# Kernel tuning notes

Measured on AMD Instinct MI355X. Metric: run time of the kernel, lower is better.

## Reference

```python
import jax, jax.numpy as jnp
import numpy as np

B, NODES, VOCAB, EMB, GIN_DIM, E_PER = 4096, 32, 100, 64, 64, 512
N = B * NODES            # total nodes in batched graph
LN_EPS = 1e-5


def setup_inputs() -> dict:
    key = jax.random.key(0)
    ks = jax.random.split(key, 12)
    x = jax.random.randint(ks[0], (B, NODES - 1), 0, VOCAB)
    los = jax.random.randint(ks[1], (B,), 0, 37)
    # intra-graph edges with per-graph node offsets -> flat batched edge_index [2, B*E_PER]
    src = jax.random.randint(ks[2], (B, E_PER), 0, NODES)
    dst = jax.random.randint(ks[3], (B, E_PER), 0, NODES)
    off = (jnp.arange(B) * NODES)[:, None]
    edge_index = jnp.stack([(src + off).reshape(-1), (dst + off).reshape(-1)])

    def w(k, shape, fan_in):
        return jax.random.normal(k, shape, dtype=jnp.float32) / np.float32(np.sqrt(fan_in))

    emb_tables = w(ks[4], (NODES, VOCAB, EMB), 1.0)  # one table per node/column
    win1 = w(ks[5], (EMB, GIN_DIM), EMB); bin1 = jnp.zeros((GIN_DIM,), jnp.float32)
    gin_g = jnp.ones((GIN_DIM,), jnp.float32); gin_b = jnp.zeros((GIN_DIM,), jnp.float32)
    win2 = w(ks[6], (GIN_DIM, GIN_DIM), GIN_DIM); bin2 = jnp.zeros((GIN_DIM,), jnp.float32)
    # hidden GIN MLP is SHARED across hidden layers (torch code reuses one nn.Sequential)
    wh1 = w(ks[7], (GIN_DIM, GIN_DIM), GIN_DIM); bh1 = jnp.zeros((GIN_DIM,), jnp.float32)
    gh_g = jnp.ones((GIN_DIM,), jnp.float32); gh_b = jnp.zeros((GIN_DIM,), jnp.float32)
    wh2 = w(ks[8], (GIN_DIM, GIN_DIM), GIN_DIM); bh2 = jnp.zeros((GIN_DIM,), jnp.float32)
    eps = jnp.zeros((3,), jnp.float32)  # trainable eps per layer, init 0
    cdim = GIN_DIM * 3
    wc1 = w(ks[9], (cdim, cdim * 2), cdim); bc1 = jnp.zeros((cdim * 2,), jnp.float32)
    wc2 = w(ks[10], (cdim * 2, 1), cdim * 2); bc2 = jnp.zeros((1,), jnp.float32)
    return dict(x=x, los=los, edge_index=edge_index, emb_tables=emb_tables,
                win1=win1, bin1=bin1, gin_g=gin_g, gin_b=gin_b, win2=win2, bin2=bin2,
                wh1=wh1, bh1=bh1, gh_g=gh_g, gh_b=gh_b, wh2=wh2, bh2=bh2,
                eps=eps, wc1=wc1, bc1=bc1, wc2=wc2, bc2=bc2)


def _ln(z, g, b):
    mu = z.mean(-1, keepdims=True)
    var = ((z - mu) ** 2).mean(-1, keepdims=True)
    return (z - mu) * jax.lax.rsqrt(var + LN_EPS) * g + b


def _gin_layer(h, src, dst, eps, W1, b1, g, be, W2, b2):
    # sum-aggregate neighbors: out_i = (1+eps)*h_i + sum_{(j,i) in E} h_j
    agg = jax.ops.segment_sum(h[src], dst, num_segments=N)
    z = (1.0 + eps) * h + agg
    z = jax.nn.relu(_ln(z @ W1 + b1, g, be))
    return z @ W2 + b2


def reference(x, los, edge_index, emb_tables, win1, bin1, gin_g, gin_b, win2, bin2,
              wh1, bh1, gh_g, gh_b, wh2, bh2, eps, wc1, bc1, wc2, bc2):
    xf = jnp.concatenate([x, los[:, None]], axis=1)        # [B, NODES]
    h = emb_tables[jnp.arange(NODES)[None, :], xf]         # per-column embedding lookup -> [B, NODES, EMB]
    h = h.reshape(N, EMB)
    src, dst = edge_index[0], edge_index[1]
    h1 = _gin_layer(h, src, dst, eps[0], win1, bin1, gin_g, gin_b, win2, bin2)
    h2 = _gin_layer(h1, src, dst, eps[1], wh1, bh1, gh_g, gh_b, wh2, bh2)
    h3 = _gin_layer(h2, src, dst, eps[2], wh1, bh1, gh_g, gh_b, wh2, bh2)
    pooled = jnp.concatenate([t.reshape(B, NODES, -1).sum(axis=1) for t in (h1, h2, h3)], axis=1)  # [B, 192]
    return jax.nn.relu(pooled @ wc1 + bc1) @ wc2 + bc2     # [B, 1]
```

## Files before the change

### kernel.cpp

```cpp
#include <hip/hip_runtime.h>

#define NBATCH 4096
#define NNODE  32
#define NVOCAB 100
#define DIM    64
#define EPG    512
#define HSTR   68
#define LN_EPS 1e-5f
#define CDIM   192
#define C2DIM  384

#define WS_WFRAG_OFF   0
#define WS_WC1_OFF     65536
#define WS_POOL_OFF    360448

typedef float          f32x4  __attribute__((ext_vector_type(4)));
typedef unsigned int   u32x4  __attribute__((ext_vector_type(4)));
typedef __bf16         bf16x8 __attribute__((ext_vector_type(8)));

__device__ __forceinline__ float4 ldg4(const float* __restrict__ p) {
    return *reinterpret_cast<const float4*>(p);
}
__device__ __forceinline__ unsigned short f2bf(float f) {
    return __builtin_bit_cast(unsigned short, static_cast<__bf16>(f));
}
__device__ __forceinline__ float bf2f(unsigned short h) {
    return static_cast<float>(__builtin_bit_cast(__bf16, h));
}
__device__ __forceinline__ unsigned int pk2(float a, float b) {
    return (unsigned int)f2bf(a) | ((unsigned int)f2bf(b) << 16);
}
__device__ __forceinline__ unsigned int pk2lo(float a, float b, unsigned int hi) {
    const float ra = a - bf2f((unsigned short)(hi & 0xffff));
    const float rb = b - bf2f((unsigned short)(hi >> 16));
    return pk2(ra, rb);
}
__device__ __forceinline__ bf16x8 as_bf(u32x4 v) {
    return __builtin_bit_cast(bf16x8, v);
}
#define MFMA(a, b, c) __builtin_amdgcn_mfma_f32_16x16x32_bf16(as_bf(a), as_bf(b), (c), 0, 0, 0)

extern "C" __global__ void __launch_bounds__(256)
prep_w_kernel(const float* __restrict__ win1, const float* __restrict__ win2,
              const float* __restrict__ wh1,  const float* __restrict__ wh2,
              const float* __restrict__ wc1,
              unsigned short* __restrict__ wsb, unsigned short* __restrict__ wc1f)
{
    const int blk = blockIdx.x;
    if (blk < 4) {
        const float* Ws[4] = {win1, win2, wh1, wh2};
        const float* W = Ws[blk];
        unsigned short* hi = wsb + blk * 8192;
        unsigned short* lo = hi + 4096;
        for (int f = threadIdx.x; f < 512; f += 256) {
            const int s = f >> 8, n = (f >> 6) & 3, l = f & 63;
            const int g = l >> 4, c = l & 15, col = n * 16 + c;
            unsigned int uh[4], ul[4];
            #pragma unroll
            for (int j2 = 0; j2 < 4; ++j2) {
                const float a = W[(s * 32 + g * 8 + j2 * 2)     * DIM + col];
                const float b = W[(s * 32 + g * 8 + j2 * 2 + 1) * DIM + col];
                uh[j2] = pk2(a, b);
                ul[j2] = pk2lo(a, b, uh[j2]);
            }
            *(u32x4*)(hi + f * 8) = (u32x4){uh[0], uh[1], uh[2], uh[3]};
            *(u32x4*)(lo + f * 8) = (u32x4){ul[0], ul[1], ul[2], ul[3]};
        }
    } else {
        unsigned short* hi = wc1f;
        unsigned short* lo = wc1f + 6 * 24 * 64 * 8;
        const int base = (blk - 4) * 768;
        for (int i = 0; i < 3; ++i) {
            const int e = base + i * 256 + threadIdx.x;
            const int s = e / (24 * 64), rem = e % (24 * 64);
            const int n = rem >> 6, l = rem & 63;
            const int col = n * 16 + (l & 15);
            const int k0 = s * 32 + (l >> 4) * 8;
            unsigned int uh[4], ul[4];
            #pragma unroll
            for (int j2 = 0; j2 < 4; ++j2) {
                const float a = wc1[(k0 + j2 * 2)     * C2DIM + col];
                const float b = wc1[(k0 + j2 * 2 + 1) * C2DIM + col];
                uh[j2] = pk2(a, b);
                ul[j2] = pk2lo(a, b, uh[j2]);
            }
            *(u32x4*)(hi + e * 8) = (u32x4){uh[0], uh[1], uh[2], uh[3]};
            *(u32x4*)(lo + e * 8) = (u32x4){ul[0], ul[1], ul[2], ul[3]};
        }
    }
}

extern "C" __global__ void __launch_bounds__(256, 4)
gin_fused_kernel(const int* __restrict__ x, const int* __restrict__ los,
                 const int* __restrict__ eidx,
                 const float* __restrict__ emb,
                 const float* __restrict__ bin1,
                 const float* __restrict__ gin_g, const float* __restrict__ gin_b,
                 const float* __restrict__ bin2,
                 const float* __restrict__ bh1,
                 const float* __restrict__ gh_g, const float* __restrict__ gh_b,
                 const float* __restrict__ bh2,
                 const float* __restrict__ epsv,
                 const unsigned short* __restrict__ wsb,
                 float* __restrict__ pooled_ws)
{
    __shared__ __align__(16) float S[4 * NNODE * HSTR];

    const int t  = threadIdx.x;
    const int wv = t >> 6;
    const int l  = t & 63;
    const int b  = blockIdx.x * 4 + wv;
    float* scr = &S[wv * NNODE * HSTR];
    const int lc = l & 15;
    const int lg = l >> 4;

    int* cnt = (int*)scr;
    #pragma unroll
    for (int i = 0; i < 16; ++i) cnt[l + 64 * i] = 0;
    {
        const int ebase = b * EPG;
        const int goff  = b * NNODE;
        #pragma unroll
        for (int i = 0; i < 8; ++i) {
            const int e = ebase + l + 64 * i;
            const int sN = eidx[e] - goff;
            const int dN = eidx[NBATCH * EPG + e] - goff;
            atomicAdd(&cnt[dN * NNODE + sN], 1);
        }
    }
    u32x4 adjf[2];
    #pragma unroll
    for (int m = 0; m < 2; ++m) {
        const int4 a0 = *(const int4*)&cnt[(m * 16 + lc) * NNODE + lg * 8];
        const int4 a1 = *(const int4*)&cnt[(m * 16 + lc) * NNODE + lg * 8 + 4];
        adjf[m] = (u32x4){ pk2((float)a0.x, (float)a0.y), pk2((float)a0.z, (float)a0.w),
                           pk2((float)a1.x, (float)a1.y), pk2((float)a1.z, (float)a1.w) };
    }
    {
        const int node = l >> 1;
        const int idx = (node < NNODE - 1) ? x[b * (NNODE - 1) + node] : los[b];
        const float* er = emb + ((size_t)(node * NVOCAB + idx)) * DIM + (l & 1) * 32;
        float* sr = scr + node * HSTR + (l & 1) * 32;
        #pragma unroll
        for (int i = 0; i < 8; ++i)
            *reinterpret_cast<float4*>(sr + i * 4) = ldg4(er + i * 4);
    }

    f32x4 acc[2][4];
    u32x4 azh[2][2], azl[2][2];

    for (int ly = 0; ly < 3; ++ly) {
        const float* B1 = ly ? bh1  : bin1;
        const float* Gg = ly ? gh_g : gin_g;
        const float* Gb = ly ? gh_b : gin_b;
        const float* B2 = ly ? bh2  : bin2;
        const unsigned short* W1f = wsb + (ly ? 2 : 0) * 8192;
        const unsigned short* W2f = wsb + (ly ? 3 : 1) * 8192;
        const float sc = 1.0f + epsv[ly];

        #pragma unroll
        for (int m = 0; m < 2; ++m)
            #pragma unroll
            for (int n = 0; n < 4; ++n)
                #pragma unroll
                for (int r = 0; r < 4; ++r)
                    acc[m][n][r] = sc * scr[(m * 16 + lg * 4 + r) * HSTR + n * 16 + lc];
        #pragma unroll
        for (int n = 0; n < 4; ++n) {
            float h[8];
            #pragma unroll
            for (int j = 0; j < 8; ++j) h[j] = scr[(lg * 8 + j) * HSTR + n * 16 + lc];
            u32x4 hh = (u32x4){ pk2(h[0],h[1]), pk2(h[2],h[3]), pk2(h[4],h[5]), pk2(h[6],h[7]) };
            u32x4 hl = (u32x4){ pk2lo(h[0],h[1],hh[0]), pk2lo(h[2],h[3],hh[1]),
                                pk2lo(h[4],h[5],hh[2]), pk2lo(h[6],h[7],hh[3]) };
            #pragma unroll
            for (int m = 0; m < 2; ++m) {
                acc[m][n] = MFMA(adjf[m], hh, acc[m][n]);
                acc[m][n] = MFMA(adjf[m], hl, acc[m][n]);
            }
        }

        #pragma unroll
        for (int m = 0; m < 2; ++m)
            #pragma unroll
            for (int n = 0; n < 4; ++n)
                #pragma unroll
                for (int r = 0; r < 4; ++r)
                    scr[(m * 16 + lg * 4 + r) * HSTR + n * 16 + lc] = acc[m][n][r];
        #pragma unroll
        for (int m = 0; m < 2; ++m)
            #pragma unroll
            for (int s = 0; s < 2; ++s) {
                const float4 v0 = *(const float4*)&scr[(m * 16 + lc) * HSTR + s * 32 + lg * 8];
                const float4 v1 = *(const float4*)&scr[(m * 16 + lc) * HSTR + s * 32 + lg * 8 + 4];
                azh[m][s] = (u32x4){ pk2(v0.x,v0.y), pk2(v0.z,v0.w), pk2(v1.x,v1.y), pk2(v1.z,v1.w) };
                azl[m][s] = (u32x4){ pk2lo(v0.x,v0.y,azh[m][s][0]), pk2lo(v0.z,v0.w,azh[m][s][1]),
                                     pk2lo(v1.x,v1.y,azh[m][s][2]), pk2lo(v1.z,v1.w,azh[m][s][3]) };
            }
        #pragma unroll
        for (int m = 0; m < 2; ++m)
            #pragma unroll
            for (int n = 0; n < 4; ++n)
                acc[m][n] = (f32x4){0.f, 0.f, 0.f, 0.f};
        #pragma unroll
        for (int n = 0; n < 4; ++n)
            #pragma unroll
            for (int s = 0; s < 2; ++s) {
                const u32x4 wh = *(const u32x4*)(W1f +        ((s * 4 + n) * 64 + l) * 8);
                const u32x4 wl = *(const u32x4*)(W1f + 4096 + ((s * 4 + n) * 64 + l) * 8);
                #pragma unroll
                for (int m = 0; m < 2; ++m) {
                    acc[m][n] = MFMA(azh[m][s], wh, acc[m][n]);
                    acc[m][n] = MFMA(azh[m][s], wl, acc[m][n]);
                    acc[m][n] = MFMA(azl[m][s], wh, acc[m][n]);
                }
            }

        {
            float bv[4], gg[4], gb[4];
            #pragma unroll
            for (int n = 0; n < 4; ++n) { bv[n] = B1[n * 16 + lc]; gg[n] = Gg[n * 16 + lc]; gb[n] = Gb[n * 16 + lc]; }
            #pragma unroll
            for (int m = 0; m < 2; ++m)
                #pragma unroll
                for (int r = 0; r < 4; ++r) {
                    float a0 = acc[m][0][r] + bv[0], a1 = acc[m][1][r] + bv[1];
                    float a2 = acc[m][2][r] + bv[2], a3 = acc[m][3][r] + bv[3];
                    float s1 = a0 + a1 + a2 + a3;
                    float s2 = a0 * a0 + a1 * a1 + a2 * a2 + a3 * a3;
                    s1 += __shfl_xor(s1, 1); s1 += __shfl_xor(s1, 2);
                    s1 += __shfl_xor(s1, 4); s1 += __shfl_xor(s1, 8);
                    s2 += __shfl_xor(s2, 1); s2 += __shfl_xor(s2, 2);
                    s2 += __shfl_xor(s2, 4); s2 += __shfl_xor(s2, 8);
                    const float mu  = s1 * (1.0f / 64.0f);
                    const float var = s2 * (1.0f / 64.0f) - mu * mu;
                    const float inv = rsqrtf(var + LN_EPS);
                    acc[m][0][r] = fmaxf((a0 - mu) * inv * gg[0] + gb[0], 0.f);
                    acc[m][1][r] = fmaxf((a1 - mu) * inv * gg[1] + gb[1], 0.f);
                    acc[m][2][r] = fmaxf((a2 - mu) * inv * gg[2] + gb[2], 0.f);
                    acc[m][3][r] = fmaxf((a3 - mu) * inv * gg[3] + gb[3], 0.f);
                }
        }

        #pragma unroll
        for (int m = 0; m < 2; ++m)
            #pragma unroll
            for (int n = 0; n < 4; ++n)
                #pragma unroll
                for (int r = 0; r < 4; ++r)
                    scr[(m * 16 + lg * 4 + r) * HSTR + n * 16 + lc] = acc[m][n][r];
        #pragma unroll
        for (int m = 0; m < 2; ++m)
            #pragma unroll
            for (int s = 0; s < 2; ++s) {
                const float4 v0 = *(const float4*)&scr[(m * 16 + lc) * HSTR + s * 32 + lg * 8];
                const float4 v1 = *(const float4*)&scr[(m * 16 + lc) * HSTR + s * 32 + lg * 8 + 4];
                azh[m][s] = (u32x4){ pk2(v0.x,v0.y), pk2(v0.z,v0.w), pk2(v1.x,v1.y), pk2(v1.z,v1.w) };
                azl[m][s] = (u32x4){ pk2lo(v0.x,v0.y,azh[m][s][0]), pk2lo(v0.z,v0.w,azh[m][s][1]),
                                     pk2lo(v1.x,v1.y,azh[m][s][2]), pk2lo(v1.z,v1.w,azh[m][s][3]) };
            }
        #pragma unroll
        for (int m = 0; m < 2; ++m)
            #pragma unroll
            for (int n = 0; n < 4; ++n)
                acc[m][n] = (f32x4){0.f, 0.f, 0.f, 0.f};
        #pragma unroll
        for (int n = 0; n < 4; ++n)
            #pragma unroll
            for (int s = 0; s < 2; ++s) {
                const u32x4 wh = *(const u32x4*)(W2f +        ((s * 4 + n) * 64 + l) * 8);
                const u32x4 wl = *(const u32x4*)(W2f + 4096 + ((s * 4 + n) * 64 + l) * 8);
                #pragma unroll
                for (int m = 0; m < 2; ++m) {
                    acc[m][n] = MFMA(azh[m][s], wh, acc[m][n]);
                    acc[m][n] = MFMA(azh[m][s], wl, acc[m][n]);
                    acc[m][n] = MFMA(azl[m][s], wh, acc[m][n]);
                }
            }
        #pragma unroll
        for (int n = 0; n < 4; ++n) {
            const float bb = B2[n * 16 + lc];
            #pragma unroll
            for (int m = 0; m < 2; ++m)
                #pragma unroll
                for (int r = 0; r < 4; ++r)
                    acc[m][n][r] += bb;
        }
        #pragma unroll
        for (int m = 0; m < 2; ++m)
            #pragma unroll
            for (int n = 0; n < 4; ++n)
                #pragma unroll
                for (int r = 0; r < 4; ++r)
                    scr[(m * 16 + lg * 4 + r) * HSTR + n * 16 + lc] = acc[m][n][r];
        #pragma unroll
        for (int n = 0; n < 4; ++n) {
            float p = 0.f;
            #pragma unroll
            for (int m = 0; m < 2; ++m)
                #pragma unroll
                for (int r = 0; r < 4; ++r) p += acc[m][n][r];
            p += __shfl_xor(p, 16);
            p += __shfl_xor(p, 32);
            if (l < 16)
                pooled_ws[(size_t)b * CDIM + ly * DIM + n * 16 + l] = p;
        }
    }
}

extern "C" __global__ void __launch_bounds__(256)
classifier_kernel(const float* __restrict__ pooled_ws,
                  const unsigned short* __restrict__ wc1f,
                  const float* __restrict__ bc1, const float* __restrict__ wc2,
                  const float* __restrict__ bc2, float* __restrict__ out)
{
    #define PSTR 196
    __shared__ __align__(16) float P[16 * PSTR];
    __shared__ __align__(16) unsigned int afh[6 * 64 * 4];
    __shared__ __align__(16) unsigned int afl[6 * 64 * 4];
    __shared__ float rsum[4][16];

    const int b = blockIdx.x;
    const int t = threadIdx.x;
    const int l = t & 63;
    const int w = t >> 6;
    const unsigned short* wc1lo = wc1f + 73728;

    for (int i = t; i < 16 * 48; i += 256) {
        const int row = i / 48, q = i % 48;
        const float4 v = ldg4(pooled_ws + ((size_t)(b * 16 + row)) * CDIM + q * 4);
        *reinterpret_cast<float4*>(&P[row * PSTR + q * 4]) = v;
    }
    __syncthreads();

    for (int e = t; e < 6 * 64; e += 256) {
        const int s = e >> 6, ll = e & 63;
        const int row = ll & 15;
        const int k0 = s * 32 + (ll >> 4) * 8;
        const float4 v0 = *reinterpret_cast<const float4*>(&P[row * PSTR + k0]);
        const float4 v1 = *reinterpret_cast<const float4*>(&P[row * PSTR + k0 + 4]);
        const float y[8] = { v0.x, v0.y, v0.z, v0.w, v1.x, v1.y, v1.z, v1.w };
        unsigned int uh[4], ul[4];
        #pragma unroll
        for (int j2 = 0; j2 < 4; ++j2) {
            uh[j2] = pk2(y[j2 * 2], y[j2 * 2 + 1]);
            ul[j2] = pk2lo(y[j2 * 2], y[j2 * 2 + 1], uh[j2]);
        }
        *reinterpret_cast<u32x4*>(&afh[e * 4]) = (u32x4){uh[0], uh[1], uh[2], uh[3]};
        *reinterpret_cast<u32x4*>(&afl[e * 4]) = (u32x4){ul[0], ul[1], ul[2], ul[3]};
    }
    __syncthreads();

    float part[4] = {0.f, 0.f, 0.f, 0.f};
    for (int nt = 0; nt < 6; ++nt) {
        const int n = w * 6 + nt;
        f32x4 acc = {0.f, 0.f, 0.f, 0.f};
        #pragma unroll
        for (int s = 0; s < 6; ++s) {
            const u32x4 ah = *(const u32x4*)&afh[(s * 64 + l) * 4];
            const u32x4 al = *(const u32x4*)&afl[(s * 64 + l) * 4];
            const u32x4 bh = *(const u32x4*)&wc1f [((s * 24 + n) * 64 + l) * 8];
            const u32x4 bl = *(const u32x4*)&wc1lo[((s * 24 + n) * 64 + l) * 8];
            acc = MFMA(ah, bh, acc);
            acc = MFMA(ah, bl, acc);
            acc = MFMA(al, bh, acc);
        }
        const int col = n * 16 + (l & 15);
        const float bias = bc1[col], w2 = wc2[col];
        #pragma unroll
        for (int r = 0; r < 4; ++r)
            part[r] += fmaxf(acc[r] + bias, 0.f) * w2;
    }
    #pragma unroll
    for (int r = 0; r < 4; ++r) {
        part[r] += __shfl_xor(part[r], 1);
        part[r] += __shfl_xor(part[r], 2);
        part[r] += __shfl_xor(part[r], 4);
        part[r] += __shfl_xor(part[r], 8);
    }
    if ((l & 15) == 0) {
        const int g = l >> 4;
        #pragma unroll
        for (int r = 0; r < 4; ++r) rsum[w][g * 4 + r] = part[r];
    }
    __syncthreads();
    if (t < 16)
        out[b * 16 + t] = rsum[0][t] + rsum[1][t] + rsum[2][t] + rsum[3][t] + bc2[0];
}

extern "C" void kernel_launch(void* const* d_in, const int* in_sizes, int n_in,
                              void* d_out, int out_size, void* d_ws, size_t ws_size,
                              hipStream_t stream)
{
    const int*   x     = (const int*)d_in[0];
    const int*   los   = (const int*)d_in[1];
    const int*   eidx  = (const int*)d_in[2];
    const float* emb   = (const float*)d_in[3];
    const float* win1  = (const float*)d_in[4];
    const float* bin1  = (const float*)d_in[5];
    const float* gin_g = (const float*)d_in[6];
    const float* gin_b = (const float*)d_in[7];
    const float* win2  = (const float*)d_in[8];
    const float* bin2  = (const float*)d_in[9];
    const float* wh1   = (const float*)d_in[10];
    const float* bh1   = (const float*)d_in[11];
    const float* gh_g  = (const float*)d_in[12];
    const float* gh_b  = (const float*)d_in[13];
    const float* wh2   = (const float*)d_in[14];
    const float* bh2   = (const float*)d_in[15];
    const float* epsv  = (const float*)d_in[16];
    const float* wc1   = (const float*)d_in[17];
    const float* bc1   = (const float*)d_in[18];
    const float* wc2   = (const float*)d_in[19];
    const float* bc2   = (const float*)d_in[20];
    float* out = (float*)d_out;

    unsigned short* wsb      = (unsigned short*)((char*)d_ws + WS_WFRAG_OFF);
    unsigned short* wc1f     = (unsigned short*)((char*)d_ws + WS_WC1_OFF);
    float*          pooledws = (float*)((char*)d_ws + WS_POOL_OFF);

    hipLaunchKernelGGL(prep_w_kernel, dim3(16), dim3(256), 0, stream,
                       win1, win2, wh1, wh2, wc1, wsb, wc1f);
    hipLaunchKernelGGL(gin_fused_kernel, dim3(NBATCH / 4), dim3(256), 0, stream,
                       x, los, eidx, emb, bin1, gin_g, gin_b, bin2,
                       bh1, gh_g, gh_b, bh2, epsv,
                       (const unsigned short*)wsb, pooledws);
    hipLaunchKernelGGL(classifier_kernel, dim3(NBATCH / 16), dim3(256), 0, stream,
                       (const float*)pooledws, (const unsigned short*)wc1f,
                       bc1, wc2, bc2, out);
}
```

Baseline: 62.37 us.

## Fold second GIN linear into next layer's first linear and classifier weights

Precomputes W2·W1 products (win2·wh1, wh2·wh1) and folded bias vectors in the prep kernel, and exploits linearity of aggregation so each layer applies the fused weight before neighbor aggregation. This removes one 64x64 MFMA matmul per layer from the per-graph kernel. Pooling now stores pre-W2 activations, so W2 and its bias are folded into the classifier weights (wc1) and bias (32·b2·wc1). The cost is extra prep-kernel work and some numerical reordering from the folded products.

New measurement: 66.78 us. 1.07x slower.

```diff
diff --git a/kernel.cpp b/kernel.cpp
--- a/kernel.cpp
+++ b/kernel.cpp
@@ -11,8 +11,10 @@
 #define C2DIM  384
 
 #define WS_WFRAG_OFF   0
-#define WS_WC1_OFF     65536
-#define WS_POOL_OFF    360448
+#define WS_B21_OFF     49152
+#define WS_WCF_OFF     65536
+#define WS_BCE_OFF     360448
+#define WS_POOL_OFF    364544
 
 typedef float          f32x4  __attribute__((ext_vector_type(4)));
 typedef unsigned int   u32x4  __attribute__((ext_vector_type(4)));
@@ -43,49 +45,108 @@
 extern "C" __global__ void __launch_bounds__(256)
 prep_w_kernel(const float* __restrict__ win1, const float* __restrict__ win2,
               const float* __restrict__ wh1,  const float* __restrict__ wh2,
-              const float* __restrict__ wc1,
-              unsigned short* __restrict__ wsb, unsigned short* __restrict__ wc1f)
+              const float* __restrict__ wc1,  const float* __restrict__ bin2,
+              const float* __restrict__ bh2,  const float* __restrict__ bc1,
+              unsigned short* __restrict__ wsb, unsigned short* __restrict__ wcf,
+              float* __restrict__ b21, float* __restrict__ bce)
 {
-    const int blk = blockIdx.x;
-    if (blk < 4) {
-        const float* Ws[4] = {win1, win2, wh1, wh2};
-        const float* W = Ws[blk];
+    __shared__ float sh[12288];
+    const int blk = blockIdx.x, t = threadIdx.x;
+
+    if (blk < 3) {
+        float* C = sh + 4096;
+        if (blk == 0) {
+            for (int i = t; i < 1024; i += 256)
+                *(float4*)&C[i * 4] = ldg4(win1 + i * 4);
+        } else {
+            const float* A2 = (blk == 1) ? win2 : wh2;
+            const float* bb = (blk == 1) ? bin2 : bh2;
+            float* Bm = sh;
+            for (int i = t; i < 1024; i += 256)
+                *(float4*)&Bm[i * 4] = ldg4(wh1 + i * 4);
+            __syncthreads();
+            const int r = t >> 2, cb = (t & 3) * 16;
+            float av[16];
+            #pragma unroll
+            for (int c = 0; c < 16; ++c) av[c] = 0.f;
+            for (int k = 0; k < 64; ++k) {
+                const float a = A2[r * 64 + k];
+                #pragma unroll
+                for (int c = 0; c < 16; ++c) av[c] = fmaf(a, Bm[k * 64 + cb + c], av[c]);
+            }
+            #pragma unroll
+            for (int c = 0; c < 16; ++c) C[r * 64 + cb + c] = av[c];
+            if (t < 64) {
+                float s = 0.f;
+                for (int k = 0; k < 64; ++k) s = fmaf(bb[k], Bm[k * 64 + t], s);
+                b21[(blk - 1) * 64 + t] = s;
+            }
+        }
+        __syncthreads();
         unsigned short* hi = wsb + blk * 8192;
         unsigned short* lo = hi + 4096;
-        for (int f = threadIdx.x; f < 512; f += 256) {
-            const int s = f >> 8, n = (f >> 6) & 3, l = f & 63;
-            const int g = l >> 4, c = l & 15, col = n * 16 + c;
+        for (int f = t; f < 512; f += 256) {
+            const int s = f >> 8, n = (f >> 6) & 3, ll = f & 63;
+            const int g = ll >> 4, col = n * 16 + (ll & 15);
             unsigned int uh[4], ul[4];
             #pragma unroll
             for (int j2 = 0; j2 < 4; ++j2) {
-                const float a = W[(s * 32 + g * 8 + j2 * 2)     * DIM + col];
-                const float b = W[(s * 32 + g * 8 + j2 * 2 + 1) * DIM + col];
-                uh[j2] = pk2(a, b);
-                ul[j2] = pk2lo(a, b, uh[j2]);
+                const float a  = C[(s * 32 + g * 8 + j2 * 2)     * 64 + col];
+                const float bq = C[(s * 32 + g * 8 + j2 * 2 + 1) * 64 + col];
+                uh[j2] = pk2(a, bq);
+                ul[j2] = pk2lo(a, bq, uh[j2]);
             }
             *(u32x4*)(hi + f * 8) = (u32x4){uh[0], uh[1], uh[2], uh[3]};
             *(u32x4*)(lo + f * 8) = (u32x4){ul[0], ul[1], ul[2], ul[3]};
         }
-    } else {
-        unsigned short* hi = wc1f;
-        unsigned short* lo = wc1f + 6 * 24 * 64 * 8;
-        const int base = (blk - 4) * 768;
-        for (int i = 0; i < 3; ++i) {
-            const int e = base + i * 256 + threadIdx.x;
-            const int s = e / (24 * 64), rem = e % (24 * 64);
-            const int n = rem >> 6, l = rem & 63;
-            const int col = n * 16 + (l & 15);
-            const int k0 = s * 32 + (l >> 4) * 8;
+    } else if (blk < 15) {
+        const int chunk = blk - 3;
+        float* wc1c = sh;
+        float* C2   = sh + 6144;
+        for (int i = t; i < 1536; i += 256) {
+            const int row = i >> 3, q = i & 7;
+            *(float4*)&wc1c[row * 32 + q * 4] = ldg4(wc1 + (size_t)row * C2DIM + chunk * 32 + q * 4);
+        }
+        __syncthreads();
+        for (int o = t; o < 6144; o += 256) {
+            const int r = o >> 5, c = o & 31;
+            const float* A2 = (r < 64) ? win2 : wh2;
+            const int rr = r & 63, kb = (r >> 6) * 64;
+            float s = 0.f;
+            for (int k = 0; k < 64; ++k)
+                s = fmaf(A2[rr * 64 + k], wc1c[(kb + k) * 32 + c], s);
+            C2[r * 32 + c] = s;
+        }
+        __syncthreads();
+        unsigned short* hi = wcf;
+        unsigned short* lo = wcf + 73728;
+        for (int i = t; i < 768; i += 256) {
+            const int s = i / 128, rem = i % 128;
+            const int nl = rem >> 6, ll = rem & 63;
+            const int n = chunk * 2 + nl;
+            const int e = (s * 24 + n) * 64 + ll;
+            const int cl = nl * 16 + (ll & 15);
+            const int k0 = s * 32 + (ll >> 4) * 8;
             unsigned int uh[4], ul[4];
             #pragma unroll
             for (int j2 = 0; j2 < 4; ++j2) {
-                const float a = wc1[(k0 + j2 * 2)     * C2DIM + col];
-                const float b = wc1[(k0 + j2 * 2 + 1) * C2DIM + col];
-                uh[j2] = pk2(a, b);
-                ul[j2] = pk2lo(a, b, uh[j2]);
+                const float a  = C2[(k0 + j2 * 2)     * 32 + cl];
+                const float bq = C2[(k0 + j2 * 2 + 1) * 32 + cl];
+                uh[j2] = pk2(a, bq);
+                ul[j2] = pk2lo(a, bq, uh[j2]);
             }
             *(u32x4*)(hi + e * 8) = (u32x4){uh[0], uh[1], uh[2], uh[3]};
             *(u32x4*)(lo + e * 8) = (u32x4){ul[0], ul[1], ul[2], ul[3]};
+        }
+    } else {
+        for (int j = t; j < C2DIM; j += 256) {
+            float s = 0.f;
+            for (int k = 0; k < 64; ++k) {
+                s = fmaf(bin2[k], wc1[(size_t)k * C2DIM + j], s);
+                s = fmaf(bh2[k],  wc1[(size_t)(64 + k) * C2DIM + j], s);
+                s = fmaf(bh2[k],  wc1[(size_t)(128 + k) * C2DIM + j], s);
+            }
+            bce[j] = bc1[j] + 32.0f * s;
         }
     }
 }
@@ -96,12 +157,11 @@
                  const float* __restrict__ emb,
                  const float* __restrict__ bin1,
                  const float* __restrict__ gin_g, const float* __restrict__ gin_b,
-                 const float* __restrict__ bin2,
                  const float* __restrict__ bh1,
                  const float* __restrict__ gh_g, const float* __restrict__ gh_b,
-                 const float* __restrict__ bh2,
                  const float* __restrict__ epsv,
                  const unsigned short* __restrict__ wsb,
+                 const float* __restrict__ b21,
                  float* __restrict__ pooled_ws)
 {
     __shared__ __align__(16) float S[4 * NNODE * HSTR];
@@ -149,44 +209,22 @@
     f32x4 acc[2][4];
     u32x4 azh[2][2], azl[2][2];
 
-    for (int ly = 0; ly < 3; ++ly) {
-        const float* B1 = ly ? bh1  : bin1;
-        const float* Gg = ly ? gh_g : gin_g;
-        const float* Gb = ly ? gh_b : gin_b;
-        const float* B2 = ly ? bh2  : bin2;
-        const unsigned short* W1f = wsb + (ly ? 2 : 0) * 8192;
-        const unsigned short* W2f = wsb + (ly ? 3 : 1) * 8192;
-        const float sc = 1.0f + epsv[ly];
-
-        #pragma unroll
-        for (int m = 0; m < 2; ++m)
-            #pragma unroll
-            for (int n = 0; n < 4; ++n)
-                #pragma unroll
-                for (int r = 0; r < 4; ++r)
-                    acc[m][n][r] = sc * scr[(m * 16 + lg * 4 + r) * HSTR + n * 16 + lc];
-        #pragma unroll
-        for (int n = 0; n < 4; ++n) {
-            float h[8];
-            #pragma unroll
-            for (int j = 0; j < 8; ++j) h[j] = scr[(lg * 8 + j) * HSTR + n * 16 + lc];
-            u32x4 hh = (u32x4){ pk2(h[0],h[1]), pk2(h[2],h[3]), pk2(h[4],h[5]), pk2(h[6],h[7]) };
-            u32x4 hl = (u32x4){ pk2lo(h[0],h[1],hh[0]), pk2lo(h[2],h[3],hh[1]),
-                                pk2lo(h[4],h[5],hh[2]), pk2lo(h[6],h[7],hh[3]) };
-            #pragma unroll
-            for (int m = 0; m < 2; ++m) {
-                acc[m][n] = MFMA(adjf[m], hh, acc[m][n]);
-                acc[m][n] = MFMA(adjf[m], hl, acc[m][n]);
-            }
-        }
-
-        #pragma unroll
-        for (int m = 0; m < 2; ++m)
-            #pragma unroll
-            for (int n = 0; n < 4; ++n)
-                #pragma unroll
-                for (int r = 0; r < 4; ++r)
-                    scr[(m * 16 + lg * 4 + r) * HSTR + n * 16 + lc] = acc[m][n][r];
+    for (int st = 0; st < 3; ++st) {
+        const unsigned short* Wf = wsb + st * 8192;
+        const float* bpost = st ? bh1  : bin1;
+        const float* Gg    = st ? gh_g : gin_g;
+        const float* Gb    = st ? gh_b : gin_b;
+        const float sc = 1.0f + epsv[st];
+
+        if (st) {
+            #pragma unroll
+            for (int m = 0; m < 2; ++m)
+                #pragma unroll
+                for (int n = 0; n < 4; ++n)
+                    #pragma unroll
+                    for (int r = 0; r < 4; ++r)
+                        scr[(m * 16 + lg * 4 + r) * HSTR + n * 16 + lc] = acc[m][n][r];
+        }
         #pragma unroll
         for (int m = 0; m < 2; ++m)
             #pragma unroll
@@ -198,16 +236,18 @@
                                      pk2lo(v1.x,v1.y,azh[m][s][2]), pk2lo(v1.z,v1.w,azh[m][s][3]) };
             }
         #pragma unroll
-        for (int m = 0; m < 2; ++m)
-            #pragma unroll
-            for (int n = 0; n < 4; ++n)
-                acc[m][n] = (f32x4){0.f, 0.f, 0.f, 0.f};
+        for (int n = 0; n < 4; ++n) {
+            const float bp = st ? b21[(st - 1) * 64 + n * 16 + lc] : 0.f;
+            #pragma unroll
+            for (int m = 0; m < 2; ++m)
+                acc[m][n] = (f32x4){bp, bp, bp, bp};
+        }
         #pragma unroll
         for (int n = 0; n < 4; ++n)
             #pragma unroll
             for (int s = 0; s < 2; ++s) {
-                const u32x4 wh = *(const u32x4*)(W1f +        ((s * 4 + n) * 64 + l) * 8);
-                const u32x4 wl = *(const u32x4*)(W1f + 4096 + ((s * 4 + n) * 64 + l) * 8);
+                const u32x4 wh = *(const u32x4*)(Wf +        ((s * 4 + n) * 64 + l) * 8);
+                const u32x4 wl = *(const u32x4*)(Wf + 4096 + ((s * 4 + n) * 64 + l) * 8);
                 #pragma unroll
                 for (int m = 0; m < 2; ++m) {
                     acc[m][n] = MFMA(azh[m][s], wh, acc[m][n]);
@@ -215,17 +255,46 @@
                     acc[m][n] = MFMA(azl[m][s], wh, acc[m][n]);
                 }
             }
-
+        #pragma unroll
+        for (int m = 0; m < 2; ++m)
+            #pragma unroll
+            for (int n = 0; n < 4; ++n)
+                #pragma unroll
+                for (int r = 0; r < 4; ++r)
+                    scr[(m * 16 + lg * 4 + r) * HSTR + n * 16 + lc] = acc[m][n][r];
+        #pragma unroll
+        for (int n = 0; n < 4; ++n) {
+            const float bq = bpost[n * 16 + lc];
+            #pragma unroll
+            for (int m = 0; m < 2; ++m)
+                #pragma unroll
+                for (int r = 0; r < 4; ++r)
+                    acc[m][n][r] = sc * acc[m][n][r] + bq;
+        }
+        #pragma unroll
+        for (int n = 0; n < 4; ++n) {
+            float h[8];
+            #pragma unroll
+            for (int j = 0; j < 8; ++j) h[j] = scr[(lg * 8 + j) * HSTR + n * 16 + lc];
+            const u32x4 hh = (u32x4){ pk2(h[0],h[1]), pk2(h[2],h[3]), pk2(h[4],h[5]), pk2(h[6],h[7]) };
+            const u32x4 hl = (u32x4){ pk2lo(h[0],h[1],hh[0]), pk2lo(h[2],h[3],hh[1]),
+                                      pk2lo(h[4],h[5],hh[2]), pk2lo(h[6],h[7],hh[3]) };
+            #pragma unroll
+            for (int m = 0; m < 2; ++m) {
+                acc[m][n] = MFMA(adjf[m], hh, acc[m][n]);
+                acc[m][n] = MFMA(adjf[m], hl, acc[m][n]);
+            }
+        }
         {
-            float bv[4], gg[4], gb[4];
-            #pragma unroll
-            for (int n = 0; n < 4; ++n) { bv[n] = B1[n * 16 + lc]; gg[n] = Gg[n * 16 + lc]; gb[n] = Gb[n * 16 + lc]; }
+            float gg[4], gb[4];
+            #pragma unroll
+            for (int n = 0; n < 4; ++n) { gg[n] = Gg[n * 16 + lc]; gb[n] = Gb[n * 16 + lc]; }
             #pragma unroll
             for (int m = 0; m < 2; ++m)
                 #pragma unroll
                 for (int r = 0; r < 4; ++r) {
-                    float a0 = acc[m][0][r] + bv[0], a1 = acc[m][1][r] + bv[1];
-                    float a2 = acc[m][2][r] + bv[2], a3 = acc[m][3][r] + bv[3];
+                    float a0 = acc[m][0][r], a1 = acc[m][1][r];
+                    float a2 = acc[m][2][r], a3 = acc[m][3][r];
                     float s1 = a0 + a1 + a2 + a3;
                     float s2 = a0 * a0 + a1 * a1 + a2 * a2 + a3 * a3;
                     s1 += __shfl_xor(s1, 1); s1 += __shfl_xor(s1, 2);
@@ -241,58 +310,6 @@
                     acc[m][3][r] = fmaxf((a3 - mu) * inv * gg[3] + gb[3], 0.f);
                 }
         }
-
-        #pragma unroll
-        for (int m = 0; m < 2; ++m)
-            #pragma unroll
-            for (int n = 0; n < 4; ++n)
-                #pragma unroll
-                for (int r = 0; r < 4; ++r)
-                    scr[(m * 16 + lg * 4 + r) * HSTR + n * 16 + lc] = acc[m][n][r];
-        #pragma unroll
-        for (int m = 0; m < 2; ++m)
-            #pragma unroll
-            for (int s = 0; s < 2; ++s) {
-                const float4 v0 = *(const float4*)&scr[(m * 16 + lc) * HSTR + s * 32 + lg * 8];
-                const float4 v1 = *(const float4*)&scr[(m * 16 + lc) * HSTR + s * 32 + lg * 8 + 4];
-                azh[m][s] = (u32x4){ pk2(v0.x,v0.y), pk2(v0.z,v0.w), pk2(v1.x,v1.y), pk2(v1.z,v1.w) };
-                azl[m][s] = (u32x4){ pk2lo(v0.x,v0.y,azh[m][s][0]), pk2lo(v0.z,v0.w,azh[m][s][1]),
-                                     pk2lo(v1.x,v1.y,azh[m][s][2]), pk2lo(v1.z,v1.w,azh[m][s][3]) };
-            }
-        #pragma unroll
-        for (int m = 0; m < 2; ++m)
-            #pragma unroll
-            for (int n = 0; n < 4; ++n)
-                acc[m][n] = (f32x4){0.f, 0.f, 0.f, 0.f};
-        #pragma unroll
-        for (int n = 0; n < 4; ++n)
-            #pragma unroll
-            for (int s = 0; s < 2; ++s) {
-                const u32x4 wh = *(const u32x4*)(W2f +        ((s * 4 + n) * 64 + l) * 8);
-                const u32x4 wl = *(const u32x4*)(W2f + 4096 + ((s * 4 + n) * 64 + l) * 8);
-                #pragma unroll
-                for (int m = 0; m < 2; ++m) {
-                    acc[m][n] = MFMA(azh[m][s], wh, acc[m][n]);
-                    acc[m][n] = MFMA(azh[m][s], wl, acc[m][n]);
-                    acc[m][n] = MFMA(azl[m][s], wh, acc[m][n]);
-                }
-            }
-        #pragma unroll
-        for (int n = 0; n < 4; ++n) {
-            const float bb = B2[n * 16 + lc];
-            #pragma unroll
-            for (int m = 0; m < 2; ++m)
-                #pragma unroll
-                for (int r = 0; r < 4; ++r)
-                    acc[m][n][r] += bb;
-        }
-        #pragma unroll
-        for (int m = 0; m < 2; ++m)
-            #pragma unroll
-            for (int n = 0; n < 4; ++n)
-                #pragma unroll
-                for (int r = 0; r < 4; ++r)
-                    scr[(m * 16 + lg * 4 + r) * HSTR + n * 16 + lc] = acc[m][n][r];
         #pragma unroll
         for (int n = 0; n < 4; ++n) {
             float p = 0.f;
@@ -303,15 +320,15 @@
             p += __shfl_xor(p, 16);
             p += __shfl_xor(p, 32);
             if (l < 16)
-                pooled_ws[(size_t)b * CDIM + ly * DIM + n * 16 + l] = p;
+                pooled_ws[(size_t)b * CDIM + st * DIM + n * 16 + l] = p;
         }
     }
 }
 
 extern "C" __global__ void __launch_bounds__(256)
 classifier_kernel(const float* __restrict__ pooled_ws,
-                  const unsigned short* __restrict__ wc1f,
-                  const float* __restrict__ bc1, const float* __restrict__ wc2,
+                  const unsigned short* __restrict__ wcf,
+                  const float* __restrict__ bce, const float* __restrict__ wc2,
                   const float* __restrict__ bc2, float* __restrict__ out)
 {
     #define PSTR 196
@@ -324,7 +341,7 @@
     const int t = threadIdx.x;
     const int l = t & 63;
     const int w = t >> 6;
-    const unsigned short* wc1lo = wc1f + 73728;
+    const unsigned short* wclo = wcf + 73728;
 
     for (int i = t; i < 16 * 48; i += 256) {
         const int row = i / 48, q = i % 48;
@@ -359,14 +376,14 @@
         for (int s = 0; s < 6; ++s) {
             const u32x4 ah = *(const u32x4*)&afh[(s * 64 + l) * 4];
             const u32x4 al = *(const u32x4*)&afl[(s * 64 + l) * 4];
-            const u32x4 bh = *(const u32x4*)&wc1f [((s * 24 + n) * 64 + l) * 8];
-            const u32x4 bl = *(const u32x4*)&wc1lo[((s * 24 + n) * 64 + l) * 8];
+            const u32x4 bh = *(const u32x4*)&wcf [((s * 24 + n) * 64 + l) * 8];
+            const u32x4 bl = *(const u32x4*)&wclo[((s * 24 + n) * 64 + l) * 8];
             acc = MFMA(ah, bh, acc);
             acc = MFMA(ah, bl, acc);
             acc = MFMA(al, bh, acc);
         }
         const int col = n * 16 + (l & 15);
-        const float bias = bc1[col], w2 = wc2[col];
+        const float bias = bce[col], w2 = wc2[col];
         #pragma unroll
         for (int r = 0; r < 4; ++r)
             part[r] += fmaxf(acc[r] + bias, 0.f) * w2;
@@ -415,17 +432,20 @@
     const float* bc2   = (const float*)d_in[20];
     float* out = (float*)d_out;
 
-    unsigned short* wsb      = (unsigned short*)((char*)d_ws + WS_WFRAG_OFF);
-    unsigned short* wc1f     = (unsigned short*)((char*)d_ws + WS_WC1_OFF);
-    float*          pooledws = (float*)((char*)d_ws + WS_POOL_OFF);
+    unsigned short* wsb = (unsigned short*)((char*)d_ws + WS_WFRAG_OFF);
+    float*          b21 = (float*)((char*)d_ws + WS_B21_OFF);
+    unsigned short* wcf = (unsigned short*)((char*)d_ws + WS_WCF_OFF);
+    float*          bce = (float*)((char*)d_ws + WS_BCE_OFF);
+    float*          cs  = (float*)((char*)d_ws + WS_POOL_OFF);
 
     hipLaunchKernelGGL(prep_w_kernel, dim3(16), dim3(256), 0, stream,
-                       win1, win2, wh1, wh2, wc1, wsb, wc1f);
+                       win1, win2, wh1, wh2, wc1, bin2, bh2, bc1,
+                       wsb, wcf, b21, bce);
     hipLaunchKernelGGL(gin_fused_kernel, dim3(NBATCH / 4), dim3(256), 0, stream,
-                       x, los, eidx, emb, bin1, gin_g, gin_b, bin2,
-                       bh1, gh_g, gh_b, bh2, epsv,
-                       (const unsigned short*)wsb, pooledws);
+                       x, los, eidx, emb, bin1, gin_g, gin_b,
+                       bh1, gh_g, gh_b, epsv,
+                       (const unsigned short*)wsb, (const float*)b21, cs);
     hipLaunchKernelGGL(classifier_kernel, dim3(NBATCH / 16), dim3(256), 0, stream,
-                       (const float*)pooledws, (const unsigned short*)wc1f,
-                       bc1, wc2, bc2, out);
-}
+                       (const float*)cs, (const unsigned short*)wcf,
+                       (const float*)bce, wc2, bc2, out);
+}
```
